# Kernel optimization log

Hardware: AMD Instinct MI355X
Metric: run time of the kernel (lower is better)

The kernel has to match this reference:

```python
import jax, jax.numpy as jnp
import numpy as np

B, S, D_IN, D_OUT = 4, 2048, 1024, 1024

def setup_inputs() -> dict:
    key = jax.random.key(0)
    kx, kq, kk, kv = jax.random.split(key, 4)
    x = jax.random.normal(kx, (B, S, D_IN), dtype=jnp.float32)
    # torch nn.Linear weight is [d_out, d_in]; we store the transposed [d_in, d_out]
    # so y = x @ W, scaled like default init to keep magnitudes sane.
    scale = 1.0 / np.sqrt(D_IN)
    Wq = jax.random.normal(kq, (D_IN, D_OUT), dtype=jnp.float32) * scale
    Wk = jax.random.normal(kk, (D_IN, D_OUT), dtype=jnp.float32) * scale
    Wv = jax.random.normal(kv, (D_IN, D_OUT), dtype=jnp.float32) * scale
    return {"x": x, "Wq": Wq, "Wk": Wk, "Wv": Wv}

def reference(x, Wq, Wk, Wv):
    b, n, _ = x.shape
    q = jnp.einsum('bnd,de->bne', x, Wq)   # [B,S,D_OUT]
    k = jnp.einsum('bnd,de->bne', x, Wk)
    v = jnp.einsum('bnd,de->bne', x, Wv)
    scores = jnp.einsum('bqe,bke->bqk', q, k) / jnp.sqrt(jnp.float32(k.shape[-1]))
    causal = jnp.triu(jnp.ones((n, n), dtype=bool), k=1)  # True above diagonal -> masked
    scores = jnp.where(causal[None, :, :], -jnp.inf, scores)
    weights = jax.nn.softmax(scores, axis=-1)
    # dropout p=0.0 (deterministic baseline) -> identity
    context = jnp.einsum('bqk,bke->bqe', weights, v)
    return context
```

## Files before the change

### kernel.cpp

```cpp
#include <hip/hip_runtime.h>
#include <hip/hip_bf16.h>

#define BB 4
#define SS 2048
#define DD 1024

typedef __attribute__((ext_vector_type(8))) short bf16x8;
typedef __attribute__((ext_vector_type(4))) float f32x4;

__device__ __forceinline__ ushort f2bf(float f) {
  unsigned u = __float_as_uint(f);
  unsigned r = (u + 0x7fffu + ((u >> 16) & 1u)) >> 16;
  return (ushort)r;
}

__device__ __forceinline__ void gload_lds16(const void* g, void* l) {
  __builtin_amdgcn_global_load_lds(
      (const __attribute__((address_space(1))) void*)g,
      (__attribute__((address_space(3))) void*)l, 16, 0, 0);
}

__global__ __launch_bounds__(256) void cast_x_kernel(const float* __restrict__ x,
                                                     ushort* __restrict__ xb) {
  const int i = blockIdx.x * 256 + threadIdx.x;
  const float4 a = ((const float4*)x)[2 * i];
  const float4 b = ((const float4*)x)[2 * i + 1];
  ushort4 o0, o1;
  o0.x = f2bf(a.x); o0.y = f2bf(a.y); o0.z = f2bf(a.z); o0.w = f2bf(a.w);
  o1.x = f2bf(b.x); o1.y = f2bf(b.y); o1.z = f2bf(b.z); o1.w = f2bf(b.w);
  ((ushort4*)xb)[2 * i] = o0;
  ((ushort4*)xb)[2 * i + 1] = o1;
}

__global__ __launch_bounds__(256) void cast_transpose_w(const float* __restrict__ W0,
                                                        const float* __restrict__ W1,
                                                        const float* __restrict__ W2,
                                                        ushort* __restrict__ Wt) {
  const float* W = blockIdx.z == 0 ? W0 : (blockIdx.z == 1 ? W1 : W2);
  ushort* O = Wt + (size_t)blockIdx.z * DD * DD;
  __shared__ ushort t[32][33];
  const int n0 = blockIdx.x * 32, k0 = blockIdx.y * 32;
  const int tx = threadIdx.x, ty = threadIdx.y;
#pragma unroll
  for (int j = 0; j < 4; j++) {
    int k = k0 + ty + j * 8;
    t[ty + j * 8][tx] = f2bf(W[(size_t)k * DD + n0 + tx]);
  }
  __syncthreads();
#pragma unroll
  for (int j = 0; j < 4; j++) {
    int n = ty + j * 8;
    O[(size_t)(n0 + n) * DD + k0 + tx] = t[tx][n];
  }
}

__global__ __launch_bounds__(256) void transpose_v(const ushort* __restrict__ V, int ldv,
                                                   ushort* __restrict__ Vt) {
  const int b = blockIdx.z;
  const ushort* Vb = V + (size_t)b * SS * ldv;
  ushort* Ob = Vt + (size_t)b * DD * SS;
  __shared__ ushort t[32][33];
  const int d0 = blockIdx.x * 32, s0 = blockIdx.y * 32;
  const int tx = threadIdx.x, ty = threadIdx.y;
#pragma unroll
  for (int j = 0; j < 4; j++) {
    int s = s0 + ty + j * 8;
    t[ty + j * 8][tx] = Vb[(size_t)s * ldv + d0 + tx];
  }
  __syncthreads();
#pragma unroll
  for (int j = 0; j < 4; j++) {
    int d = ty + j * 8;
    Ob[(size_t)(d0 + d) * SS + s0 + tx] = t[tx][d];
  }
}

template <int BM, int BN, bool TRI, bool EXPMASK, bool KCLIP, bool DIVL, bool OUT_BF16>
__global__ __launch_bounds__(512) void gemm8(const ushort* __restrict__ A, int lda, size_t strA,
                                             const ushort* __restrict__ Bt, int ldb, size_t strB,
                                             void* __restrict__ C, int ldc, size_t strC, int K) {
  constexpr int LA = BM / 64;
  constexpr int LB = BN / 64;
  constexpr int FM = BM / 32;
  constexpr int FN = BN / 64;
  int nb, mb, bz;
  if (TRI) {
    int flat = blockIdx.x + 72 * blockIdx.z;
    flat = (flat & 7) * 36 + (flat >> 3);
    bz = flat / 72;
    int i = flat % 72;
    mb = (int)((sqrtf(4.f * i + 1.f) - 1.f) * 0.5f);
    while ((mb + 1) * (mb + 2) <= i) ++mb;
    while (mb * (mb + 1) > i) --mb;
    nb = i - mb * (mb + 1);
  } else {
    nb = blockIdx.x; mb = blockIdx.y; bz = blockIdx.z;
  }
  const ushort* Ab = A + (size_t)bz * strA;
  const ushort* Bb = Bt + (size_t)bz * strB;

  __shared__ ushort lds[2][(BM + BN) * 64];

  const int tid = threadIdx.x;
  const int lane = tid & 63;
  const int wid = tid >> 6;
  const int wr = wid >> 2, wc = wid & 3;
  const int fr = lane & 15, qq = lane >> 4;
  const int sx = (fr & 7) << 4;

  int kEnd = KCLIP ? (mb + 1) * BM : K;
  if (kEnd > K) kEnd = K;
  const int NT = kEnd >> 6;

  auto stage = [&](int kt, int buf) {
    ushort* As = &lds[buf][0];
    ushort* Bs = &lds[buf][BM * 64];
    const ushort* ga = Ab + (size_t)mb * BM * lda + kt * 64;
    const ushort* gb = Bb + (size_t)nb * BN * ldb + kt * 64;
#pragma unroll
    for (int j = 0; j < LA; j++) {
      int D = (j * 512 + tid) * 16;
      int r = D >> 7;
      int cb = (D & 127) ^ ((r & 7) << 4);
      gload_lds16(ga + (size_t)r * lda + (cb >> 1), (char*)As + D);
    }
#pragma unroll
    for (int j = 0; j < LB; j++) {
      int D = (j * 512 + tid) * 16;
      int r = D >> 7;
      int cb = (D & 127) ^ ((r & 7) << 4);
      gload_lds16(gb + (size_t)r * ldb + (cb >> 1), (char*)Bs + D);
    }
  };

  stage(0, 0);
  if (NT > 1) stage(1, 1);

  f32x4 acc[FM][FN] = {};
  float lsum[FM];
#pragma unroll
  for (int i = 0; i < FM; i++) lsum[i] = 0.f;

  for (int kt = 0; kt < NT; ++kt) {
    const int cur = kt & 1;
    if (kt < NT - 1) {
      if constexpr (LA + LB == 6) asm volatile("s_waitcnt vmcnt(6)" ::: "memory");
      else if constexpr (LA + LB == 4) asm volatile("s_waitcnt vmcnt(4)" ::: "memory");
      else asm volatile("s_waitcnt vmcnt(0)" ::: "memory");
    } else {
      asm volatile("s_waitcnt vmcnt(0)" ::: "memory");
    }
    __builtin_amdgcn_s_barrier();
    __builtin_amdgcn_sched_barrier(0);

    const char* As = (const char*)&lds[cur][0];
    const char* Bs = (const char*)&lds[cur][BM * 64];
    __builtin_amdgcn_s_setprio(1);
#pragma unroll
    for (int ks = 0; ks < 2; ++ks) {
      const int kb = ks * 64 + qq * 16;
      bf16x8 a[FM], b[FN];
#pragma unroll
      for (int i = 0; i < FM; i++) {
        int r = wr * (BM / 2) + i * 16 + fr;
        a[i] = *(const bf16x8*)(As + r * 128 + (kb ^ sx));
      }
#pragma unroll
      for (int j = 0; j < FN; j++) {
        int r = wc * (BN / 4) + j * 16 + fr;
        b[j] = *(const bf16x8*)(Bs + r * 128 + (kb ^ sx));
      }
      if (DIVL && wc == 0) {
#pragma unroll
        for (int i = 0; i < FM; i++)
#pragma unroll
          for (int e = 0; e < 8; e++)
            lsum[i] += __uint_as_float((unsigned)(unsigned short)a[i][e] << 16);
      }
#pragma unroll
      for (int i = 0; i < FM; i++)
#pragma unroll
        for (int j = 0; j < FN; j++)
          acc[i][j] = __builtin_amdgcn_mfma_f32_16x16x32_bf16(a[i], b[j], acc[i][j], 0, 0, 0);
    }
    __builtin_amdgcn_s_setprio(0);
    __builtin_amdgcn_s_barrier();
    __builtin_amdgcn_sched_barrier(0);
    if (kt + 2 < NT) stage(kt + 2, cur);
  }

  __shared__ float lds_l[2][BM / 2];
  if (DIVL) {
    if (wc == 0) {
#pragma unroll
      for (int i = 0; i < FM; i++) {
        lsum[i] += __shfl_xor(lsum[i], 16);
        lsum[i] += __shfl_xor(lsum[i], 32);
      }
      if (qq == 0) {
#pragma unroll
        for (int i = 0; i < FM; i++) lds_l[wr][i * 16 + fr] = lsum[i];
      }
    }
    __syncthreads();
  }

  const int col0 = nb * BN + wc * (BN / 4) + fr;
  const int row00 = mb * BM + wr * (BM / 2) + qq * 4;
  if (OUT_BF16) {
    ushort* Cb = (ushort*)C + (size_t)bz * strC;
#pragma unroll
    for (int i = 0; i < FM; i++)
#pragma unroll
      for (int rr = 0; rr < 4; rr++) {
        const int row = row00 + i * 16 + rr;
        size_t ro = (size_t)row * ldc;
#pragma unroll
        for (int j = 0; j < FN; j++) {
          float v = acc[i][j][rr];
          if (EXPMASK) {
            v = __expf(v * 0.03125f);
            if (col0 + j * 16 > row) v = 0.f;
          }
          Cb[ro + col0 + j * 16] = f2bf(v);
        }
      }
  } else {
    float* Cb = (float*)C + (size_t)bz * strC;
#pragma unroll
    for (int i = 0; i < FM; i++)
#pragma unroll
      for (int rr = 0; rr < 4; rr++) {
        size_t ro = (size_t)(row00 + i * 16 + rr) * ldc;
        float invl = 1.f;
        if (DIVL) invl = 1.f / lds_l[wr][i * 16 + qq * 4 + rr];
#pragma unroll
        for (int j = 0; j < FN; j++) Cb[ro + col0 + j * 16] = acc[i][j][rr] * invl;
      }
  }
}

extern "C" void kernel_launch(void* const* d_in, const int* in_sizes, int n_in,
                              void* d_out, int out_size, void* d_ws, size_t ws_size,
                              hipStream_t stream) {
  const float* x = (const float*)d_in[0];
  const float* Wq = (const float*)d_in[1];
  const float* Wk = (const float*)d_in[2];
  const float* Wv = (const float*)d_in[3];

  char* ws = (char*)d_ws;
  ushort* xb = (ushort*)(ws);
  ushort* Wt = (ushort*)(ws + 16777216);
  ushort* QKV = (ushort*)(ws + 23068672);
  ushort* P = (ushort*)(ws + 73400320);
  ushort* Vt = (ushort*)(ws);

  const size_t SD = (size_t)SS * DD;
  const size_t S2 = (size_t)SS * SS;
  const size_t SQ = (size_t)SS * 3072;

  cast_x_kernel<<<(BB * SS * DD) / (256 * 8), 256, 0, stream>>>(x, xb);
  cast_transpose_w<<<dim3(DD / 32, DD / 32, 3), dim3(32, 8), 0, stream>>>(Wq, Wk, Wv, Wt);
  gemm8<256, 128, false, false, false, false, true>
      <<<dim3(3072 / 128, (BB * SS) / 256, 1), 512, 0, stream>>>(
          xb, DD, 0, Wt, DD, 0, QKV, 3072, 0, DD);
  transpose_v<<<dim3(DD / 32, SS / 32, BB), dim3(32, 8), 0, stream>>>(QKV + 2048, 3072, Vt);
  gemm8<256, 128, true, true, false, false, true><<<dim3(72, 1, BB), 512, 0, stream>>>(
      QKV, 3072, SQ, QKV + 1024, 3072, SQ, P, SS, S2, DD);
  gemm8<128, 128, false, false, true, true, false>
      <<<dim3(DD / 128, SS / 128, BB), 512, 0, stream>>>(
          P, SS, S2, Vt, SS, SD, d_out, DD, SD, SS);

  (void)in_sizes; (void)n_in; (void)out_size; (void)ws_size;
}
```

Measured before the change: 178.9 us.

## Add dedicated 256x256 QKV projection GEMM with split-K-half pipelining

Replaces the generic 256x128 gemm8 for the fused QKV projection with a specialized 256x256-tile kernel. It uses double-buffered direct-to-LDS loads split into two K-halves, an XOR-swizzled LDS layout, explicit vmcnt waits and barriers interleaving prefetch with MFMA, setprio around MFMA bursts, and a grouped block-order remap for L2 locality. The larger tile raises arithmetic intensity, but it cuts the grid to 384 blocks and uses 128KB of LDS per block, which may limit occupancy and leave the epilogue's scattered 2-byte stores uncoalesced.

```diff
diff --git a/kernel.cpp b/kernel.cpp
--- a/kernel.cpp
+++ b/kernel.cpp
@@ -18,6 +18,11 @@
   __builtin_amdgcn_global_load_lds(
       (const __attribute__((address_space(1))) void*)g,
       (__attribute__((address_space(3))) void*)l, 16, 0, 0);
+}
+
+__device__ __forceinline__ void BARSB() {
+  __builtin_amdgcn_s_barrier();
+  __builtin_amdgcn_sched_barrier(0);
 }
 
 __global__ __launch_bounds__(256) void cast_x_kernel(const float* __restrict__ x,
@@ -73,6 +78,116 @@
     int d = ty + j * 8;
     Ob[(size_t)(d0 + d) * SS + s0 + tx] = t[tx][d];
   }
+}
+
+__global__ __launch_bounds__(512, 2) void gemm256(const ushort* __restrict__ A, int lda,
+                                                  const ushort* __restrict__ Bt, int ldb,
+                                                  ushort* __restrict__ C, int ldc, int K,
+                                                  int NBCOLS) {
+  const int nwg = gridDim.x * gridDim.y;
+  int ord = blockIdx.y * gridDim.x + blockIdx.x;
+  int flat = (ord & 7) * (nwg >> 3) + (ord >> 3);
+  const int mb = flat / NBCOLS, nb = flat % NBCOLS;
+
+  __shared__ char ldsA[2][2][16384];
+  __shared__ char ldsB[2][2][16384];
+
+  const int tid = threadIdx.x;
+  const int lane = tid & 63, wid = tid >> 6;
+  const int wr = wid >> 2, wc = wid & 3;
+  const int fr = lane & 15, qq = lane >> 4;
+  const int kxor = ((qq ^ ((fr >> 1) & 3)) << 4);
+
+  const int srcE = (((tid & 3) ^ ((tid >> 3) & 3)) << 3);
+  const ushort* Ag_t = A + (size_t)(mb * 256 + (tid >> 2)) * lda + srcE;
+  const ushort* Bg_t = Bt + (size_t)(nb * 256 + (tid >> 2)) * ldb + srcE;
+
+  const int NT = K >> 6;
+
+  auto stA = [&](int buf, int kh, int kt) {
+#pragma unroll
+    for (int j = 0; j < 2; j++)
+      gload_lds16(Ag_t + (size_t)(j * 128) * lda + kt * 64 + kh * 32,
+                  &ldsA[buf][kh][(j * 512 + tid) * 16]);
+  };
+  auto stB = [&](int buf, int kh, int kt) {
+#pragma unroll
+    for (int j = 0; j < 2; j++)
+      gload_lds16(Bg_t + (size_t)(j * 128) * ldb + kt * 64 + kh * 32,
+                  &ldsB[buf][kh][(j * 512 + tid) * 16]);
+  };
+  auto ldA8 = [&](int buf, int kh, bf16x8* o) {
+#pragma unroll
+    for (int i = 0; i < 8; i++)
+      o[i] = *(const bf16x8*)(&ldsA[buf][kh][0] + ((wr * 128 + i * 16 + fr) << 6) + kxor);
+  };
+  auto ldB2 = [&](int buf, int kh, int n0, bf16x8* o) {
+#pragma unroll
+    for (int n = 0; n < 2; n++)
+      o[n] = *(const bf16x8*)(&ldsB[buf][kh][0] + ((wc * 64 + (n0 + n) * 16 + fr) << 6) + kxor);
+  };
+
+  f32x4 acc[8][4] = {};
+  bf16x8 a[8], b0[2], b1[2];
+
+#define MF16(BV, NB)                                                           \
+  do {                                                                         \
+    __builtin_amdgcn_s_setprio(1);                                             \
+    _Pragma("unroll") for (int i_ = 0; i_ < 8; i_++) {                         \
+      _Pragma("unroll") for (int n_ = 0; n_ < 2; n_++) {                       \
+        acc[i_][(NB) + n_] = __builtin_amdgcn_mfma_f32_16x16x32_bf16(          \
+            a[i_], BV[n_], acc[i_][(NB) + n_], 0, 0, 0);                       \
+      }                                                                        \
+    }                                                                          \
+    __builtin_amdgcn_s_setprio(0);                                             \
+  } while (0)
+
+  stA(0, 0, 0); stB(0, 0, 0); stA(0, 1, 0); stB(0, 1, 0);
+  __builtin_amdgcn_sched_barrier(0);
+  asm volatile("s_waitcnt vmcnt(4)" ::: "memory");
+  BARSB();
+
+  for (int kt = 0; kt < NT; ++kt) {
+    const int cur = kt & 1, nxt = cur ^ 1;
+    const bool pf = (kt + 1 < NT);
+    ldA8(cur, 0, a);
+    ldB2(cur, 0, 0, b0);
+    if (pf) stA(nxt, 0, kt + 1);
+    MF16(b0, 0);
+    BARSB();
+    ldB2(cur, 0, 2, b1);
+    if (pf) stB(nxt, 0, kt + 1);
+    MF16(b1, 2);
+    __builtin_amdgcn_sched_barrier(0);
+    if (pf) asm volatile("s_waitcnt vmcnt(4)" ::: "memory");
+    else    asm volatile("s_waitcnt vmcnt(0)" ::: "memory");
+    BARSB();
+    ldA8(cur, 1, a);
+    ldB2(cur, 1, 0, b0);
+    if (pf) stA(nxt, 1, kt + 1);
+    MF16(b0, 0);
+    BARSB();
+    ldB2(cur, 1, 2, b1);
+    if (pf) stB(nxt, 1, kt + 1);
+    MF16(b1, 2);
+    __builtin_amdgcn_sched_barrier(0);
+    if (pf) {
+      asm volatile("s_waitcnt vmcnt(4)" ::: "memory");
+      BARSB();
+    }
+  }
+#undef MF16
+
+  const int col0 = nb * 256 + wc * 64 + fr;
+  const int row00 = mb * 256 + wr * 128 + qq * 4;
+#pragma unroll
+  for (int i = 0; i < 8; i++)
+#pragma unroll
+    for (int rr = 0; rr < 4; rr++) {
+      size_t ro = (size_t)(row00 + i * 16 + rr) * ldc;
+#pragma unroll
+      for (int n = 0; n < 4; n++) C[ro + col0 + n * 16] = f2bf(acc[i][n][rr]);
+    }
 }
 
 template <int BM, int BN, bool TRI, bool EXPMASK, bool KCLIP, bool DIVL, bool OUT_BF16>
@@ -261,9 +376,7 @@
 
   cast_x_kernel<<<(BB * SS * DD) / (256 * 8), 256, 0, stream>>>(x, xb);
   cast_transpose_w<<<dim3(DD / 32, DD / 32, 3), dim3(32, 8), 0, stream>>>(Wq, Wk, Wv, Wt);
-  gemm8<256, 128, false, false, false, false, true>
-      <<<dim3(3072 / 128, (BB * SS) / 256, 1), 512, 0, stream>>>(
-          xb, DD, 0, Wt, DD, 0, QKV, 3072, 0, DD);
+  gemm256<<<dim3(12, 32, 1), 512, 0, stream>>>(xb, DD, Wt, DD, QKV, 3072, DD, 12);
   transpose_v<<<dim3(DD / 32, SS / 32, BB), dim3(32, 8), 0, stream>>>(QKV + 2048, 3072, Vt);
   gemm8<256, 128, true, true, false, false, true><<<dim3(72, 1, BB), 512, 0, stream>>>(
       QKV, 3072, SQ, QKV + 1024, 3072, SQ, P, SS, S2, DD);
```

After: 178.7 us. About the same (-0.1%).
